# Performance work log

Hardware: AMD Instinct MI355X
Metric: run time of the kernel (lower is better)

The kernel has to match this reference:

```python
import jax, jax.numpy as jnp
import numpy as np
import math

BT, N, D, H = 16, 1024, 128, 8
HD = D // H


def setup_inputs() -> dict:
    key = jax.random.key(0)
    ks = jax.random.split(key, 12)
    s = 1.0 / math.sqrt(D)
    return {
        "x": jax.random.normal(ks[0], (BT, N, D), dtype=jnp.float32),
        "adj": jax.random.uniform(ks[1], (BT, N, N), dtype=jnp.float32),
        "Wq": jax.random.normal(ks[2], (D, D), dtype=jnp.float32) * s,
        "bq": jax.random.normal(ks[3], (D,), dtype=jnp.float32) * 0.01,
        "Wk": jax.random.normal(ks[4], (D, D), dtype=jnp.float32) * s,
        "bk": jax.random.normal(ks[5], (D,), dtype=jnp.float32) * 0.01,
        "Wv": jax.random.normal(ks[6], (D, D), dtype=jnp.float32) * s,
        "bv": jax.random.normal(ks[7], (D,), dtype=jnp.float32) * 0.01,
        "Wo": jax.random.normal(ks[8], (D, D), dtype=jnp.float32) * s,
        "bo": jax.random.normal(ks[9], (D,), dtype=jnp.float32) * 0.01,
    }


def reference(x, adj, Wq, bq, Wk, bk, Wv, bv, Wo, bo):
    bt, n, d = x.shape
    # projections (torch Linear: x @ W.T + b), split into heads -> (BT,H,N,HD)
    q = (x @ Wq.T + bq).reshape(bt, n, H, HD).transpose(0, 2, 1, 3)
    k = (x @ Wk.T + bk).reshape(bt, n, H, HD).transpose(0, 2, 1, 3)
    v = (x @ Wv.T + bv).reshape(bt, n, H, HD).transpose(0, 2, 1, 3)
    scores = jnp.einsum('bhnd,bhmd->bhnm', q, k) / math.sqrt(HD)  # (BT,H,N,N)
    mask = (adj == 0)[:, None, :, :]  # (BT,1,N,N)
    scores = jnp.where(mask, -jnp.inf, scores)
    attn = jax.nn.softmax(scores, axis=-1)
    attn = attn * adj[:, None, :, :]  # reweight by continuous causal strength
    attn = attn / (attn.sum(axis=-1, keepdims=True) + 1e-8)  # renormalize
    ctx = jnp.einsum('bhnm,bhmd->bhnd', attn, v)  # (BT,H,N,HD)
    ctx = ctx.transpose(0, 2, 1, 3).reshape(bt, n, d)
    return ctx @ Wo.T + bo
```

## Files before the change

### kernel.cpp

```cpp
#include <hip/hip_runtime.h>
#include <hip/hip_bf16.h>

#define BTC 16
#define NC 1024
#define DC 128
#define HC 8
#define HDC 16

typedef __attribute__((ext_vector_type(8))) short bf16x8;
typedef __attribute__((ext_vector_type(4))) float f32x4;
typedef __attribute__((ext_vector_type(4))) short short4v;

#if __has_builtin(__builtin_amdgcn_exp2f)
#define EXP2F(x) __builtin_amdgcn_exp2f(x)
#else
#define EXP2F(x) exp2f(x)
#endif

#define QSCALE 0.36067376022224085f

union PK2 { short4v s4; __hip_bfloat162 h2[2]; };
union PK8 { bf16x8 v; short s[8]; __hip_bfloat162 h2[4]; };

static __device__ inline short f2bf(float f) {
    unsigned u = __builtin_bit_cast(unsigned, f);
    u += 0x7fffu + ((u >> 16) & 1u);
    return (short)(u >> 16);
}

static __device__ inline bf16x8 zero8() {
    PK8 f;
#pragma unroll
    for (int j = 0; j < 8; ++j) f.s[j] = 0;
    return f.v;
}

__global__ __launch_bounds__(256)
void prep_kernel(const float* __restrict__ x,
                 const float* __restrict__ Wq, const float* __restrict__ Wk,
                 const float* __restrict__ Wv, const float* __restrict__ Wo,
                 short* __restrict__ xbf, short* __restrict__ Wbf)
{
    int gid  = blockIdx.x * 256 + threadIdx.x;
    int base = gid * 4;
    const float* src;
    short* dst;
    if (base < 2097152) {
        src = x + base; dst = xbf + base;
    } else {
        int idx = base - 2097152;
        int w   = idx >> 14;
        int off = idx & 16383;
        src = ((w == 0) ? Wq : (w == 1) ? Wk : (w == 2) ? Wv : Wo) + off;
        dst = Wbf + w * 16384 + off;
    }
    float4 v = *(const float4*)src;
    PK2 pk;
    pk.h2[0] = __float22bfloat162_rn(make_float2(v.x, v.y));
    pk.h2[1] = __float22bfloat162_rn(make_float2(v.z, v.w));
    *(short4v*)dst = pk.s4;
}

__global__ __launch_bounds__(256)
void proj_qkv(const short* __restrict__ xbf, const short* __restrict__ Wbf,
              const float* __restrict__ bq, const float* __restrict__ bk,
              const float* __restrict__ bv,
              short* __restrict__ qo, short* __restrict__ ko, short* __restrict__ vto)
{
    const int y = blockIdx.y;
    const short* W = Wbf + y * 16384;
    const float* bias = (y == 0) ? bq : (y == 1) ? bk : bv;
    const float scale = (y == 0) ? QSCALE : 1.0f;

    const int tid  = threadIdx.x;
    const int wave = tid >> 6;
    const int lane = tid & 63;
    const int l15  = lane & 15;
    const int quad = lane >> 4;
    const int rowA = blockIdx.x * 64 + wave * 16;

    f32x4 acc[8];
#pragma unroll
    for (int t = 0; t < 8; ++t) acc[t] = (f32x4){0.f, 0.f, 0.f, 0.f};

#pragma unroll
    for (int kk = 0; kk < DC; kk += 32) {
        bf16x8 Af = *(const bf16x8*)&xbf[(size_t)(rowA + l15) * DC + kk + quad * 8];
#pragma unroll
        for (int t = 0; t < 8; ++t) {
            bf16x8 Bf = *(const bf16x8*)&W[(t * 16 + l15) * DC + kk + quad * 8];
            acc[t] = __builtin_amdgcn_mfma_f32_16x16x32_bf16(Af, Bf, acc[t], 0, 0, 0);
        }
    }

#pragma unroll
    for (int t = 0; t < 8; ++t) {
        int c = t * 16 + l15;
        float b = bias[c];
#pragma unroll
        for (int r = 0; r < 4; ++r) {
            int row = rowA + quad * 4 + r;
            float val = (acc[t][r] + b) * scale;
            if (y == 2)
                vto[(size_t)(row >> 10) * 131072 + (size_t)c * 1024 + (row & 1023)] = f2bf(val);
            else
                ((y == 0) ? qo : ko)[(size_t)row * DC + c] = f2bf(val);
        }
    }
}

__global__ __launch_bounds__(256)
void proj_out(const short* __restrict__ cbf, const short* __restrict__ Wobf,
              const float* __restrict__ bo, float* __restrict__ out)
{
    const int tid  = threadIdx.x;
    const int wave = tid >> 6;
    const int lane = tid & 63;
    const int l15  = lane & 15;
    const int quad = lane >> 4;
    const int rowA = blockIdx.x * 64 + wave * 16;

    f32x4 acc[8];
#pragma unroll
    for (int t = 0; t < 8; ++t) acc[t] = (f32x4){0.f, 0.f, 0.f, 0.f};

#pragma unroll
    for (int kk = 0; kk < DC; kk += 32) {
        bf16x8 Af = *(const bf16x8*)&cbf[(size_t)(rowA + l15) * DC + kk + quad * 8];
#pragma unroll
        for (int t = 0; t < 8; ++t) {
            bf16x8 Bf = *(const bf16x8*)&Wobf[(t * 16 + l15) * DC + kk + quad * 8];
            acc[t] = __builtin_amdgcn_mfma_f32_16x16x32_bf16(Af, Bf, acc[t], 0, 0, 0);
        }
    }

#pragma unroll
    for (int t = 0; t < 8; ++t) {
        int c = t * 16 + l15;
        float b = bo[c];
#pragma unroll
        for (int r = 0; r < 4; ++r) {
            int row = rowA + quad * 4 + r;
            out[(size_t)row * DC + c] = acc[t][r] + b;
        }
    }
}

__global__ __launch_bounds__(512)
void attn_kernel(const short* __restrict__ qb, const short* __restrict__ kb,
                 const short* __restrict__ vt, const float* __restrict__ adj,
                 short* __restrict__ cb)
{
    __shared__ float As[2][32 * 36];
    __shared__ short Ps[8 * 32 * 40];

    const int tid  = threadIdx.x;
    const int wave = tid >> 6;
    const int lane = tid & 63;
    const int l15  = lane & 15;
    const int quad = lane >> 4;
    const int bt   = blockIdx.y;
    const int qt0  = blockIdx.x * 32;
    const int h    = wave;

    const size_t xb = (size_t)bt * NC * DC;
    const size_t ab = (size_t)bt * NC * NC;

    bf16x8 Bq[2];
#pragma unroll
    for (int s = 0; s < 2; ++s)
        Bq[s] = (quad < 2)
            ? *(const bf16x8*)&qb[xb + (size_t)(qt0 + s * 16 + l15) * DC + h * HDC + quad * 8]
            : zero8();

    PK8 ones;
#pragma unroll
    for (int j = 0; j < 8; ++j) ones.s[j] = (short)0x3F80;

    f32x4 Cc[2], Cw[2];
#pragma unroll
    for (int s = 0; s < 2; ++s) {
        Cc[s] = (f32x4){0.f, 0.f, 0.f, 0.f};
        Cw[s] = (f32x4){0.f, 0.f, 0.f, 0.f};
    }

    const int arow = tid >> 4;
    const int acol = (tid & 15) * 2;
    const float* aptr = adj + ab + (size_t)(qt0 + arow) * NC + acol;
    float2 ar = *(const float2*)aptr;
    int p = 0;
    short* Pw = Ps + wave * 1280;

    for (int jt = 0; jt < NC; jt += 32) {
        *(float2*)&As[p][arow * 36 + acol] = ar;
        if (jt + 32 < NC) ar = *(const float2*)(aptr + jt + 32);
        __syncthreads();

        bf16x8 Ak[2];
#pragma unroll
        for (int g = 0; g < 2; ++g)
            Ak[g] = (quad < 2)
                ? *(const bf16x8*)&kb[xb + (size_t)(jt + g * 16 + l15) * DC + h * HDC + quad * 8]
                : zero8();
        bf16x8 Bv = *(const bf16x8*)&vt[((size_t)bt * DC + h * HDC + l15) * NC + jt + quad * 8];

        const f32x4 z4 = (f32x4){0.f, 0.f, 0.f, 0.f};
        f32x4 S[2][2];
#pragma unroll
        for (int s = 0; s < 2; ++s)
#pragma unroll
            for (int g = 0; g < 2; ++g)
                S[s][g] = __builtin_amdgcn_mfma_f32_16x16x32_bf16(Ak[g], Bq[s], z4, 0, 0, 0);

#pragma unroll
        for (int s = 0; s < 2; ++s)
#pragma unroll
            for (int g = 0; g < 2; ++g) {
                float4 a4 = *(const float4*)&As[p][(s * 16 + l15) * 36 + g * 16 + quad * 4];
                float p0 = EXP2F(S[s][g][0]) * a4.x;
                float p1 = EXP2F(S[s][g][1]) * a4.y;
                float p2 = EXP2F(S[s][g][2]) * a4.z;
                float p3 = EXP2F(S[s][g][3]) * a4.w;
                PK2 pk;
                pk.h2[0] = __float22bfloat162_rn(make_float2(p0, p1));
                pk.h2[1] = __float22bfloat162_rn(make_float2(p2, p3));
                *(short4v*)&Pw[(s * 16 + l15) * 40 + g * 16 + quad * 4] = pk.s4;
            }
        __builtin_amdgcn_wave_barrier();

#pragma unroll
        for (int s = 0; s < 2; ++s) {
            bf16x8 Ap = *(const bf16x8*)&Pw[(s * 16 + l15) * 40 + quad * 8];
            Cc[s] = __builtin_amdgcn_mfma_f32_16x16x32_bf16(Ap, Bv, Cc[s], 0, 0, 0);
            Cw[s] = __builtin_amdgcn_mfma_f32_16x16x32_bf16(Ap, ones.v, Cw[s], 0, 0, 0);
        }
        p ^= 1;
    }

#pragma unroll
    for (int s = 0; s < 2; ++s)
#pragma unroll
        for (int r = 0; r < 4; ++r) {
            float den = Cw[s][r];
            float rcp = den > 0.f ? 1.f / den : 0.f;
            int row = qt0 + s * 16 + quad * 4 + r;
            cb[xb + (size_t)row * DC + h * HDC + l15] = f2bf(Cc[s][r] * rcp);
        }
}

extern "C" void kernel_launch(void* const* d_in, const int* in_sizes, int n_in,
                              void* d_out, int out_size, void* d_ws, size_t ws_size,
                              hipStream_t stream)
{
    const float* x   = (const float*)d_in[0];
    const float* adj = (const float*)d_in[1];
    const float* Wq  = (const float*)d_in[2];
    const float* bq  = (const float*)d_in[3];
    const float* Wk  = (const float*)d_in[4];
    const float* bk  = (const float*)d_in[5];
    const float* Wv  = (const float*)d_in[6];
    const float* bv  = (const float*)d_in[7];
    const float* Wo  = (const float*)d_in[8];
    const float* bo  = (const float*)d_in[9];
    float* out = (float*)d_out;

    const size_t tok = (size_t)BTC * NC * DC;
    short* xbf  = (short*)d_ws;
    short* Wbf  = xbf  + tok;
    short* qbuf = Wbf  + 65536;
    short* kbuf = qbuf + tok;
    short* vt   = kbuf + tok;
    short* cbuf = vt   + tok;

    prep_kernel<<<2112, 256, 0, stream>>>(x, Wq, Wk, Wv, Wo, xbf, Wbf);

    dim3 pgrid(256, 3);
    proj_qkv<<<pgrid, 256, 0, stream>>>(xbf, Wbf, bq, bk, bv, qbuf, kbuf, vt);

    dim3 agrid(32, 16);
    attn_kernel<<<agrid, 512, 0, stream>>>(qbuf, kbuf, vt, adj, cbuf);

    proj_out<<<256, 256, 0, stream>>>(cbuf, Wbf + 3 * 16384, bo, out);
}
```

Measured before the change: 178.8 us.

## Fuse bf16 conversion into projections and output projection into attention kernel

Drops the separate fp32-to-bf16 prep kernel by converting x and weights on the fly inside the QKV projection. Fuses the output projection into the attention kernel by staging the per-tile context in shared memory and multiplying it by Wo there, which removes the context buffer round-trip and two kernel launches. The attention inner loop now uses 32x32x16 MFMA for the scores, where the old 16x16 form zero-padded half of each operand, and stages adjacency 128 columns per block barrier instead of 32. The cost is more shared memory and register use per block, plus redundant fp32 weight loads and conversions in every block.

```diff
diff --git a/kernel.cpp b/kernel.cpp
--- a/kernel.cpp
+++ b/kernel.cpp
@@ -7,9 +7,10 @@
 #define HC 8
 #define HDC 16
 
-typedef __attribute__((ext_vector_type(8))) short bf16x8;
-typedef __attribute__((ext_vector_type(4))) float f32x4;
-typedef __attribute__((ext_vector_type(4))) short short4v;
+typedef __attribute__((ext_vector_type(8)))  short bf16x8;
+typedef __attribute__((ext_vector_type(4)))  float f32x4;
+typedef __attribute__((ext_vector_type(16))) float f32x16;
+typedef __attribute__((ext_vector_type(4)))  short short4v;
 
 #if __has_builtin(__builtin_amdgcn_exp2f)
 #define EXP2F(x) __builtin_amdgcn_exp2f(x)
@@ -28,47 +29,24 @@
     return (short)(u >> 16);
 }
 
-static __device__ inline bf16x8 zero8() {
+static __device__ inline bf16x8 pack8f(float4 a, float4 b) {
     PK8 f;
-#pragma unroll
-    for (int j = 0; j < 8; ++j) f.s[j] = 0;
+    f.h2[0] = __float22bfloat162_rn(make_float2(a.x, a.y));
+    f.h2[1] = __float22bfloat162_rn(make_float2(a.z, a.w));
+    f.h2[2] = __float22bfloat162_rn(make_float2(b.x, b.y));
+    f.h2[3] = __float22bfloat162_rn(make_float2(b.z, b.w));
     return f.v;
 }
 
 __global__ __launch_bounds__(256)
-void prep_kernel(const float* __restrict__ x,
-                 const float* __restrict__ Wq, const float* __restrict__ Wk,
-                 const float* __restrict__ Wv, const float* __restrict__ Wo,
-                 short* __restrict__ xbf, short* __restrict__ Wbf)
-{
-    int gid  = blockIdx.x * 256 + threadIdx.x;
-    int base = gid * 4;
-    const float* src;
-    short* dst;
-    if (base < 2097152) {
-        src = x + base; dst = xbf + base;
-    } else {
-        int idx = base - 2097152;
-        int w   = idx >> 14;
-        int off = idx & 16383;
-        src = ((w == 0) ? Wq : (w == 1) ? Wk : (w == 2) ? Wv : Wo) + off;
-        dst = Wbf + w * 16384 + off;
-    }
-    float4 v = *(const float4*)src;
-    PK2 pk;
-    pk.h2[0] = __float22bfloat162_rn(make_float2(v.x, v.y));
-    pk.h2[1] = __float22bfloat162_rn(make_float2(v.z, v.w));
-    *(short4v*)dst = pk.s4;
-}
-
-__global__ __launch_bounds__(256)
-void proj_qkv(const short* __restrict__ xbf, const short* __restrict__ Wbf,
-              const float* __restrict__ bq, const float* __restrict__ bk,
-              const float* __restrict__ bv,
+void proj_qkv(const float* __restrict__ x,
+              const float* __restrict__ Wq, const float* __restrict__ bq,
+              const float* __restrict__ Wk, const float* __restrict__ bk,
+              const float* __restrict__ Wv, const float* __restrict__ bv,
               short* __restrict__ qo, short* __restrict__ ko, short* __restrict__ vto)
 {
     const int y = blockIdx.y;
-    const short* W = Wbf + y * 16384;
+    const float* W    = (y == 0) ? Wq : (y == 1) ? Wk : Wv;
     const float* bias = (y == 0) ? bq : (y == 1) ? bk : bv;
     const float scale = (y == 0) ? QSCALE : 1.0f;
 
@@ -85,10 +63,12 @@
 
 #pragma unroll
     for (int kk = 0; kk < DC; kk += 32) {
-        bf16x8 Af = *(const bf16x8*)&xbf[(size_t)(rowA + l15) * DC + kk + quad * 8];
+        const float* xp = &x[(size_t)(rowA + l15) * DC + kk + quad * 8];
+        bf16x8 Af = pack8f(*(const float4*)xp, *(const float4*)(xp + 4));
 #pragma unroll
         for (int t = 0; t < 8; ++t) {
-            bf16x8 Bf = *(const bf16x8*)&W[(t * 16 + l15) * DC + kk + quad * 8];
+            const float* wp = &W[(size_t)(t * 16 + l15) * DC + kk + quad * 8];
+            bf16x8 Bf = pack8f(*(const float4*)wp, *(const float4*)(wp + 4));
             acc[t] = __builtin_amdgcn_mfma_f32_16x16x32_bf16(Af, Bf, acc[t], 0, 0, 0);
         }
     }
@@ -102,63 +82,30 @@
             int row = rowA + quad * 4 + r;
             float val = (acc[t][r] + b) * scale;
             if (y == 2)
-                vto[(size_t)(row >> 10) * 131072 + (size_t)c * 1024 + (row & 1023)] = f2bf(val);
+                vto[(size_t)(row >> 10) * (DC * NC) + (size_t)c * NC + (row & (NC - 1))] = f2bf(val);
             else
                 ((y == 0) ? qo : ko)[(size_t)row * DC + c] = f2bf(val);
         }
     }
 }
 
-__global__ __launch_bounds__(256)
-void proj_out(const short* __restrict__ cbf, const short* __restrict__ Wobf,
-              const float* __restrict__ bo, float* __restrict__ out)
+__global__ __launch_bounds__(512, 4)
+void attn_fused(const short* __restrict__ qb, const short* __restrict__ kb,
+                const short* __restrict__ vt, const float* __restrict__ adj,
+                const float* __restrict__ Wo, const float* __restrict__ bo,
+                float* __restrict__ out)
 {
+    __shared__ float As[2][32 * 132];
+    __shared__ short Ps[8][32 * 40];
+    __shared__ short Cs[32 * 136];
+
     const int tid  = threadIdx.x;
     const int wave = tid >> 6;
     const int lane = tid & 63;
     const int l15  = lane & 15;
     const int quad = lane >> 4;
-    const int rowA = blockIdx.x * 64 + wave * 16;
-
-    f32x4 acc[8];
-#pragma unroll
-    for (int t = 0; t < 8; ++t) acc[t] = (f32x4){0.f, 0.f, 0.f, 0.f};
-
-#pragma unroll
-    for (int kk = 0; kk < DC; kk += 32) {
-        bf16x8 Af = *(const bf16x8*)&cbf[(size_t)(rowA + l15) * DC + kk + quad * 8];
-#pragma unroll
-        for (int t = 0; t < 8; ++t) {
-            bf16x8 Bf = *(const bf16x8*)&Wobf[(t * 16 + l15) * DC + kk + quad * 8];
-            acc[t] = __builtin_amdgcn_mfma_f32_16x16x32_bf16(Af, Bf, acc[t], 0, 0, 0);
-        }
-    }
-
-#pragma unroll
-    for (int t = 0; t < 8; ++t) {
-        int c = t * 16 + l15;
-        float b = bo[c];
-#pragma unroll
-        for (int r = 0; r < 4; ++r) {
-            int row = rowA + quad * 4 + r;
-            out[(size_t)row * DC + c] = acc[t][r] + b;
-        }
-    }
-}
-
-__global__ __launch_bounds__(512)
-void attn_kernel(const short* __restrict__ qb, const short* __restrict__ kb,
-                 const short* __restrict__ vt, const float* __restrict__ adj,
-                 short* __restrict__ cb)
-{
-    __shared__ float As[2][32 * 36];
-    __shared__ short Ps[8 * 32 * 40];
-
-    const int tid  = threadIdx.x;
-    const int wave = tid >> 6;
-    const int lane = tid & 63;
-    const int l15  = lane & 15;
-    const int quad = lane >> 4;
+    const int l31  = lane & 31;
+    const int lh   = lane >> 5;
     const int bt   = blockIdx.y;
     const int qt0  = blockIdx.x * 32;
     const int h    = wave;
@@ -166,12 +113,7 @@
     const size_t xb = (size_t)bt * NC * DC;
     const size_t ab = (size_t)bt * NC * NC;
 
-    bf16x8 Bq[2];
-#pragma unroll
-    for (int s = 0; s < 2; ++s)
-        Bq[s] = (quad < 2)
-            ? *(const bf16x8*)&qb[xb + (size_t)(qt0 + s * 16 + l15) * DC + h * HDC + quad * 8]
-            : zero8();
+    bf16x8 Bq = *(const bf16x8*)&qb[xb + (size_t)(qt0 + l31) * DC + h * HDC + lh * 8];
 
     PK8 ones;
 #pragma unroll
@@ -185,56 +127,59 @@
     }
 
     const int arow = tid >> 4;
-    const int acol = (tid & 15) * 2;
+    const int acol = (tid & 15) * 8;
     const float* aptr = adj + ab + (size_t)(qt0 + arow) * NC + acol;
-    float2 ar = *(const float2*)aptr;
-    int p = 0;
-    short* Pw = Ps + wave * 1280;
-
-    for (int jt = 0; jt < NC; jt += 32) {
-        *(float2*)&As[p][arow * 36 + acol] = ar;
-        if (jt + 32 < NC) ar = *(const float2*)(aptr + jt + 32);
+    float4 a0 = *(const float4*)aptr;
+    float4 a1 = *(const float4*)(aptr + 4);
+
+    short* Pw = &Ps[wave][0];
+    const f32x16 z16 = {0.f,0.f,0.f,0.f,0.f,0.f,0.f,0.f,0.f,0.f,0.f,0.f,0.f,0.f,0.f,0.f};
+
+    for (int ss = 0; ss < 8; ++ss) {
+        const int p = ss & 1;
+        *(float4*)&As[p][arow * 132 + acol]     = a0;
+        *(float4*)&As[p][arow * 132 + acol + 4] = a1;
         __syncthreads();
-
-        bf16x8 Ak[2];
-#pragma unroll
-        for (int g = 0; g < 2; ++g)
-            Ak[g] = (quad < 2)
-                ? *(const bf16x8*)&kb[xb + (size_t)(jt + g * 16 + l15) * DC + h * HDC + quad * 8]
-                : zero8();
-        bf16x8 Bv = *(const bf16x8*)&vt[((size_t)bt * DC + h * HDC + l15) * NC + jt + quad * 8];
-
-        const f32x4 z4 = (f32x4){0.f, 0.f, 0.f, 0.f};
-        f32x4 S[2][2];
-#pragma unroll
-        for (int s = 0; s < 2; ++s)
-#pragma unroll
-            for (int g = 0; g < 2; ++g)
-                S[s][g] = __builtin_amdgcn_mfma_f32_16x16x32_bf16(Ak[g], Bq[s], z4, 0, 0, 0);
-
-#pragma unroll
-        for (int s = 0; s < 2; ++s)
-#pragma unroll
-            for (int g = 0; g < 2; ++g) {
-                float4 a4 = *(const float4*)&As[p][(s * 16 + l15) * 36 + g * 16 + quad * 4];
-                float p0 = EXP2F(S[s][g][0]) * a4.x;
-                float p1 = EXP2F(S[s][g][1]) * a4.y;
-                float p2 = EXP2F(S[s][g][2]) * a4.z;
-                float p3 = EXP2F(S[s][g][3]) * a4.w;
+        if (ss < 7) {
+            a0 = *(const float4*)(aptr + (ss + 1) * 128);
+            a1 = *(const float4*)(aptr + (ss + 1) * 128 + 4);
+        }
+
+        const int jt0 = ss * 128;
+        bf16x8 Kf[4], Vf[4];
+#pragma unroll
+        for (int jj = 0; jj < 4; ++jj) {
+            Kf[jj] = *(const bf16x8*)&kb[xb + (size_t)(jt0 + jj * 32 + l31) * DC + h * HDC + lh * 8];
+            Vf[jj] = *(const bf16x8*)&vt[((size_t)bt * DC + h * HDC + l15) * NC + jt0 + jj * 32 + quad * 8];
+        }
+
+#pragma unroll
+        for (int jj = 0; jj < 4; ++jj) {
+            f32x16 S = __builtin_amdgcn_mfma_f32_32x32x16_bf16(Kf[jj], Bq, z16, 0, 0, 0);
+
+#pragma unroll
+            for (int rr = 0; rr < 4; ++rr) {
+                int keyb = 8 * rr + 4 * lh;
+                float4 a4 = *(const float4*)&As[p][l31 * 132 + jj * 32 + keyb];
+                float p0 = EXP2F(S[4 * rr + 0]) * a4.x;
+                float p1 = EXP2F(S[4 * rr + 1]) * a4.y;
+                float p2 = EXP2F(S[4 * rr + 2]) * a4.z;
+                float p3 = EXP2F(S[4 * rr + 3]) * a4.w;
                 PK2 pk;
                 pk.h2[0] = __float22bfloat162_rn(make_float2(p0, p1));
                 pk.h2[1] = __float22bfloat162_rn(make_float2(p2, p3));
-                *(short4v*)&Pw[(s * 16 + l15) * 40 + g * 16 + quad * 4] = pk.s4;
+                *(short4v*)&Pw[l31 * 40 + keyb] = pk.s4;
             }
-        __builtin_amdgcn_wave_barrier();
-
-#pragma unroll
-        for (int s = 0; s < 2; ++s) {
-            bf16x8 Ap = *(const bf16x8*)&Pw[(s * 16 + l15) * 40 + quad * 8];
-            Cc[s] = __builtin_amdgcn_mfma_f32_16x16x32_bf16(Ap, Bv, Cc[s], 0, 0, 0);
-            Cw[s] = __builtin_amdgcn_mfma_f32_16x16x32_bf16(Ap, ones.v, Cw[s], 0, 0, 0);
-        }
-        p ^= 1;
+            __builtin_amdgcn_wave_barrier();
+
+#pragma unroll
+            for (int s = 0; s < 2; ++s) {
+                bf16x8 Ap = *(const bf16x8*)&Pw[(s * 16 + l15) * 40 + quad * 8];
+                Cc[s] = __builtin_amdgcn_mfma_f32_16x16x32_bf16(Ap, Vf[jj], Cc[s], 0, 0, 0);
+                Cw[s] = __builtin_amdgcn_mfma_f32_16x16x32_bf16(Ap, ones.v, Cw[s], 0, 0, 0);
+            }
+            __builtin_amdgcn_wave_barrier();
+        }
     }
 
 #pragma unroll
@@ -243,9 +188,39 @@
         for (int r = 0; r < 4; ++r) {
             float den = Cw[s][r];
             float rcp = den > 0.f ? 1.f / den : 0.f;
-            int row = qt0 + s * 16 + quad * 4 + r;
-            cb[xb + (size_t)row * DC + h * HDC + l15] = f2bf(Cc[s][r] * rcp);
-        }
+            int row = s * 16 + quad * 4 + r;
+            Cs[row * 136 + h * HDC + l15] = f2bf(Cc[s][r] * rcp);
+        }
+    __syncthreads();
+
+    const int rows0 = (wave & 1) * 16;
+    const int tbase = wave >> 1;
+    f32x4 oacc[2];
+    oacc[0] = (f32x4){0.f, 0.f, 0.f, 0.f};
+    oacc[1] = (f32x4){0.f, 0.f, 0.f, 0.f};
+
+#pragma unroll
+    for (int kk = 0; kk < DC; kk += 32) {
+        bf16x8 Ac = *(const bf16x8*)&Cs[(rows0 + l15) * 136 + kk + quad * 8];
+#pragma unroll
+        for (int ti = 0; ti < 2; ++ti) {
+            int t = tbase + ti * 4;
+            const float* wp = &Wo[(size_t)(t * 16 + l15) * DC + kk + quad * 8];
+            bf16x8 Bf = pack8f(*(const float4*)wp, *(const float4*)(wp + 4));
+            oacc[ti] = __builtin_amdgcn_mfma_f32_16x16x32_bf16(Ac, Bf, oacc[ti], 0, 0, 0);
+        }
+    }
+
+#pragma unroll
+    for (int ti = 0; ti < 2; ++ti) {
+        int c = (tbase + ti * 4) * 16 + l15;
+        float b = bo[c];
+#pragma unroll
+        for (int r = 0; r < 4; ++r) {
+            int row = qt0 + rows0 + quad * 4 + r;
+            out[((size_t)bt * NC + row) * DC + c] = oacc[ti][r] + b;
+        }
+    }
 }
 
 extern "C" void kernel_launch(void* const* d_in, const int* in_sizes, int n_in,
@@ -265,20 +240,13 @@
     float* out = (float*)d_out;
 
     const size_t tok = (size_t)BTC * NC * DC;
-    short* xbf  = (short*)d_ws;
-    short* Wbf  = xbf  + tok;
-    short* qbuf = Wbf  + 65536;
+    short* qbuf = (short*)d_ws;
     short* kbuf = qbuf + tok;
     short* vt   = kbuf + tok;
-    short* cbuf = vt   + tok;
-
-    prep_kernel<<<2112, 256, 0, stream>>>(x, Wq, Wk, Wv, Wo, xbf, Wbf);
 
     dim3 pgrid(256, 3);
-    proj_qkv<<<pgrid, 256, 0, stream>>>(xbf, Wbf, bq, bk, bv, qbuf, kbuf, vt);
-
-    dim3 agrid(32, 16);
-    attn_kernel<<<agrid, 512, 0, stream>>>(qbuf, kbuf, vt, adj, cbuf);
-
-    proj_out<<<256, 256, 0, stream>>>(cbuf, Wbf + 3 * 16384, bo, out);
-}
+    proj_qkv<<<pgrid, 256, 0, stream>>>(x, Wq, bq, Wk, bk, Wv, bv, qbuf, kbuf, vt);
+
+    dim3 agrid(NC / 32, BTC);
+    attn_fused<<<agrid, 512, 0, stream>>>(qbuf, kbuf, vt, adj, Wo, bo, out);
+}
```

After: 186.9 us. 1.05x slower.
